# Kernel tuning notes

Hardware: AMD Instinct MI355X
Metric: run time of the kernel (lower is better)

Reference implementation:

```python
import jax, jax.numpy as jnp
import numpy as np
import math

N_NODES = 50000
N_EDGES = 800000
F_IN = 32
HID = 64


def _layernorm(x, g, b, eps=1e-5):
    mu = x.mean(-1, keepdims=True)
    var = ((x - mu) ** 2).mean(-1, keepdims=True)
    return (x - mu) / jnp.sqrt(var + eps) * g + b


def _tconv(x, src, dst, Wq, bq, Wk, bk, Wv, bv, Ws, heads):
    # PyG TransformerConv (concat=True, root_weight=True, bias=False on skip)
    N = x.shape[0]
    C = Wq.shape[1] // heads
    q = (x @ Wq + bq).reshape(N, heads, C)[dst]  # [E,H,C] gathered at targets
    k = (x @ Wk + bk).reshape(N, heads, C)[src]  # [E,H,C] gathered at sources
    v = (x @ Wv + bv).reshape(N, heads, C)[src]
    scores = (q * k).sum(-1) / math.sqrt(C)      # [E,H]
    m = jax.ops.segment_max(scores, dst, num_segments=N)   # [N,H]
    p = jnp.exp(scores - m[dst])
    denom = jax.ops.segment_sum(p, dst, num_segments=N)
    alpha = p / (denom[dst] + 1e-16)             # segment softmax over in-edges
    agg = jax.ops.segment_sum(v * alpha[..., None], dst, num_segments=N)
    return agg.reshape(N, heads * C) + x @ Ws    # + skip (no bias)


def setup_inputs() -> dict:
    key = jax.random.key(0)
    ks = iter(jax.random.split(key, 64))
    def rn(shape, s=0.1):
        return jax.random.normal(next(ks), shape, jnp.float32) * s
    inp = {
        "x": rn((N_NODES, F_IN), 1.0),
        "edge_index": jax.random.randint(next(ks), (2, N_EDGES), 0, N_NODES, dtype=jnp.int32),
        "ln0_g": jnp.ones((F_IN,), jnp.float32),
        "ln0_b": jnp.zeros((F_IN,), jnp.float32),
    }
    dims = [F_IN, HID, HID]
    for l in range(3):
        d = dims[l]
        inp[f"Wq{l}"] = rn((d, HID)); inp[f"bq{l}"] = rn((HID,), 0.05)
        inp[f"Wk{l}"] = rn((d, HID)); inp[f"bk{l}"] = rn((HID,), 0.05)
        inp[f"Wv{l}"] = rn((d, HID)); inp[f"bv{l}"] = rn((HID,), 0.05)
        inp[f"Ws{l}"] = rn((d, HID))
        inp[f"g{l}"] = jnp.ones((HID,), jnp.float32)
        inp[f"b{l}"] = jnp.zeros((HID,), jnp.float32)
    inp["Wr1"] = rn((HID, HID // 2)); inp["br1"] = jnp.zeros((HID // 2,), jnp.float32)
    inp["Wr2"] = rn((HID // 2, 1));   inp["br2"] = jnp.zeros((1,), jnp.float32)
    inp["Wt1"] = rn((HID, HID // 2)); inp["bt1"] = jnp.zeros((HID // 2,), jnp.float32)
    inp["Wt2"] = rn((HID // 2, 1));   inp["bt2"] = jnp.zeros((1,), jnp.float32)
    return inp


def reference(x, edge_index, ln0_g, ln0_b,
              Wq0, bq0, Wk0, bk0, Wv0, bv0, Ws0, g0, b0,
              Wq1, bq1, Wk1, bk1, Wv1, bv1, Ws1, g1, b1,
              Wq2, bq2, Wk2, bk2, Wv2, bv2, Ws2, g2, b2,
              Wr1, br1, Wr2, br2, Wt1, bt1, Wt2, bt2):
    src, dst = edge_index[0], edge_index[1]
    h = _layernorm(x, ln0_g, ln0_b)
    layers = [
        (Wq0, bq0, Wk0, bk0, Wv0, bv0, Ws0, g0, b0, 4),
        (Wq1, bq1, Wk1, bk1, Wv1, bv1, Ws1, g1, b1, 4),
        (Wq2, bq2, Wk2, bk2, Wv2, bv2, Ws2, g2, b2, 1),
    ]
    for i, (Wq, bq, Wk, bk, Wv, bv, Ws, g, b, heads) in enumerate(layers):
        x_res = h if h.shape[-1] == HID else None
        h = _tconv(h, src, dst, Wq, bq, Wk, bk, Wv, bv, Ws, heads)
        h = _layernorm(h, g, b)
        if x_res is not None and i > 0:
            h = h + 0.1 * x_res
        if i < len(layers) - 1:
            h = jax.nn.relu(h)  # dropout is identity in eval mode
    rtt = jax.nn.relu(h @ Wr1 + br1) @ Wr2 + br2      # [N,1]
    retrans = jax.nn.relu(h @ Wt1 + bt1) @ Wt2 + bt2  # [N,1]
    return jnp.concatenate([rtt, retrans], axis=1)    # [N,2]
```

## Files before the change

### kernel.cpp

```cpp
#include <hip/hip_runtime.h>
#include <hip/hip_bf16.h>
#include <math.h>

#define N_NODES 50000
#define N_EDGES 800000
#define HID 64
#define NBK 196
#define EPB 1024
#define SB  ((N_EDGES + EPB - 1) / EPB)
#define FLAT (NBK * SB)
#define SCAN_B ((FLAT + 255) / 256)

#define QKVS0_BLKS 3125

#define LN0_BLKS   6250
#define HIST_BLKS  SB
#define WP0_BLKS   32
#define WP12_BLKS  64
#define PREP_BLKS  (LN0_BLKS + HIST_BLKS + WP0_BLKS + 2 * WP12_BLKS)

typedef __attribute__((ext_vector_type(8))) short short8;
typedef __attribute__((ext_vector_type(4))) float float4v;

__device__ __forceinline__ unsigned short f32_to_bf16_rne(float f) {
    unsigned int u = __float_as_uint(f);
    unsigned int r = u + 0x7fffu + ((u >> 16) & 1u);
    return (unsigned short)(r >> 16);
}

__device__ __forceinline__ void ln0_body(int b, int t,
        const float* __restrict__ x, const float* __restrict__ g,
        const float* __restrict__ bb, float* __restrict__ h0) {
    int lane = t & 63;
    int n = b * 8 + (t >> 6) * 2 + (lane >> 5);
    int c = lane & 31;
    float v = x[n * 32 + c];
    float s = v;
    #pragma unroll
    for (int off = 1; off < 32; off <<= 1) s += __shfl_xor(s, off);
    float mu = s * (1.0f / 32.0f);
    float d = v - mu;
    float vs = d * d;
    #pragma unroll
    for (int off = 1; off < 32; off <<= 1) vs += __shfl_xor(vs, off);
    float var = vs * (1.0f / 32.0f);
    h0[n * 32 + c] = d * rsqrtf(var + 1e-5f) * g[c] + bb[c];
}

__device__ __forceinline__ void wprep_body(int idx, int KS,
        const float* __restrict__ Wq, const float* __restrict__ Wk,
        const float* __restrict__ Wv, const float* __restrict__ Ws,
        unsigned short* __restrict__ Wp) {
    int j = idx & 7;
    int lane = (idx >> 3) & 63;
    int ts = idx >> 9;
    int s = ts % KS;
    int tile = ts / KS;
    int which = tile >> 2;
    int slice = tile & 3;
    int k = s * 32 + ((lane >> 4) * 8) + j;
    int col = slice * 16 + (lane & 15);
    const float* W = (which == 0) ? Wq : (which == 1) ? Wk : (which == 2) ? Wv : Ws;
    Wp[idx] = f32_to_bf16_rne(W[k * 64 + col]);
}

__global__ __launch_bounds__(256) void prep_kernel(
        const float* __restrict__ x, const float* __restrict__ ln0g,
        const float* __restrict__ ln0b, float* __restrict__ h0,
        const int* __restrict__ dst, int* __restrict__ ghist,
        const float* __restrict__ Wq0, const float* __restrict__ Wk0,
        const float* __restrict__ Wv0, const float* __restrict__ Ws0,
        unsigned short* __restrict__ Wp0,
        const float* __restrict__ Wq1, const float* __restrict__ Wk1,
        const float* __restrict__ Wv1, const float* __restrict__ Ws1,
        unsigned short* __restrict__ Wp1,
        const float* __restrict__ Wq2, const float* __restrict__ Wk2,
        const float* __restrict__ Wv2, const float* __restrict__ Ws2,
        unsigned short* __restrict__ Wp2) {
    __shared__ int hist[NBK];
    int b = blockIdx.x;
    int t = threadIdx.x;
    if (b < LN0_BLKS) {
        ln0_body(b, t, x, ln0g, ln0b, h0);
    } else if (b < LN0_BLKS + HIST_BLKS) {
        int i = b - LN0_BLKS;
        for (int k = t; k < NBK; k += 256) hist[k] = 0;
        __syncthreads();
        int e0 = i * EPB;
        #pragma unroll
        for (int r = 0; r < EPB / 256; r++) {
            int e = e0 + r * 256 + t;
            if (e < N_EDGES) atomicAdd(&hist[dst[e] >> 8], 1);
        }
        __syncthreads();
        for (int k = t; k < NBK; k += 256) ghist[k * SB + i] = hist[k];
    } else if (b < LN0_BLKS + HIST_BLKS + WP0_BLKS) {
        int idx = (b - LN0_BLKS - HIST_BLKS) * 256 + t;
        wprep_body(idx, 1, Wq0, Wk0, Wv0, Ws0, Wp0);
    } else if (b < LN0_BLKS + HIST_BLKS + WP0_BLKS + WP12_BLKS) {
        int idx = (b - LN0_BLKS - HIST_BLKS - WP0_BLKS) * 256 + t;
        wprep_body(idx, 2, Wq1, Wk1, Wv1, Ws1, Wp1);
    } else {
        int idx = (b - LN0_BLKS - HIST_BLKS - WP0_BLKS - WP12_BLKS) * 256 + t;
        wprep_body(idx, 2, Wq2, Wk2, Wv2, Ws2, Wp2);
    }
}

__global__ void scan1_kernel(const int* __restrict__ ghist, int* __restrict__ csum) {
    int f = blockIdx.x * 256 + threadIdx.x;
    int v = (f < FLAT) ? ghist[f] : 0;
    #pragma unroll
    for (int off = 1; off < 64; off <<= 1) v += __shfl_xor(v, off);
    __shared__ int ws[4];
    if ((threadIdx.x & 63) == 0) ws[threadIdx.x >> 6] = v;
    __syncthreads();
    if (threadIdx.x == 0) csum[blockIdx.x] = ws[0] + ws[1] + ws[2] + ws[3];
}

__global__ void scan2_kernel(const int* __restrict__ csum, int* __restrict__ coff,
                             int* __restrict__ bbase, int* __restrict__ row_ptr) {
    int lane = threadIdx.x;
    int carry = 0;
    for (int base = 0; base < SCAN_B; base += 64) {
        int i = base + lane;
        int v = (i < SCAN_B) ? csum[i] : 0;
        int incl = v;
        #pragma unroll
        for (int off = 1; off < 64; off <<= 1) {
            int tt = __shfl_up(incl, off);
            if (lane >= off) incl += tt;
        }
        if (i < SCAN_B) coff[i] = carry + incl - v;
        carry += __shfl(incl, 63);
    }
    if (lane == 0) { bbase[NBK] = N_EDGES; row_ptr[N_NODES] = N_EDGES; }
}

__global__ void scan3_kernel(const int* __restrict__ ghist, const int* __restrict__ coff,
                             int* __restrict__ goff, int* __restrict__ bbase) {
    int f = blockIdx.x * 256 + threadIdx.x;
    int lane = threadIdx.x & 63;
    int w = threadIdx.x >> 6;
    int v = (f < FLAT) ? ghist[f] : 0;
    int incl = v;
    #pragma unroll
    for (int off = 1; off < 64; off <<= 1) {
        int tt = __shfl_up(incl, off);
        if (lane >= off) incl += tt;
    }
    __shared__ int ws[4];
    if (lane == 63) ws[w] = incl;
    __syncthreads();
    int woff = 0;
    #pragma unroll
    for (int k = 0; k < 4; k++) if (k < w) woff += ws[k];
    int excl = coff[blockIdx.x] + woff + incl - v;
    if (f < FLAT) {
        goff[f] = excl;
        if (f % SB == 0) bbase[f / SB] = excl;
    }
}

template <int D>
__device__ __forceinline__ void qkvs_body(int bid, int t,
        const float* __restrict__ h,
        const unsigned short* __restrict__ Wp,
        const float* __restrict__ bq, const float* __restrict__ bk,
        const float* __restrict__ bv, float scale,
        unsigned int* __restrict__ QS, unsigned int* __restrict__ KV) {
    constexpr int KS = D / 32;
    int lane = t & 63;
    int w = t >> 6;
    int n0 = bid * 16;
    int n16 = lane & 15;
    int quad = lane >> 4;
    int col = w * 16 + n16;

    short8 afrag[KS];
    #pragma unroll
    for (int s = 0; s < KS; s++) {
        const float* hp = &h[(n0 + n16) * D + s * 32 + quad * 8];
        float4 a0 = *(const float4*)hp;
        float4 a1 = *(const float4*)(hp + 4);
        short8 af;
        af[0] = (short)f32_to_bf16_rne(a0.x);
        af[1] = (short)f32_to_bf16_rne(a0.y);
        af[2] = (short)f32_to_bf16_rne(a0.z);
        af[3] = (short)f32_to_bf16_rne(a0.w);
        af[4] = (short)f32_to_bf16_rne(a1.x);
        af[5] = (short)f32_to_bf16_rne(a1.y);
        af[6] = (short)f32_to_bf16_rne(a1.z);
        af[7] = (short)f32_to_bf16_rne(a1.w);
        afrag[s] = af;
    }

    float4v accs[4];
    #pragma unroll
    for (int which = 0; which < 4; which++) {
        float4v acc = {0.0f, 0.0f, 0.0f, 0.0f};
        int tile = which * 4 + w;
        #pragma unroll
        for (int s = 0; s < KS; s++) {
            short8 bfrag = *(const short8*)&Wp[((tile * KS + s) * 64 + lane) * 8];
            acc = __builtin_amdgcn_mfma_f32_16x16x32_bf16(afrag[s], bfrag, acc, 0, 0, 0);
        }
        accs[which] = acc;
    }

    float bqc = bq[col], bkc = bk[col], bvc = bv[col];

    #pragma unroll
    for (int r = 0; r < 4; r++) {
        int node = n0 + quad * 4 + r;
        unsigned int qw = f32_to_bf16_rne((accs[0][r] + bqc) * scale);
        unsigned int kw = f32_to_bf16_rne(accs[1][r] + bkc);
        unsigned int vw = f32_to_bf16_rne(accs[2][r] + bvc);
        unsigned int sw = f32_to_bf16_rne(accs[3][r]);
        KV[node * 64 + col] = (vw << 16) | kw;
        QS[node * 64 + col] = (sw << 16) | qw;
    }
}

template <int D>
__global__ __launch_bounds__(256) void qkvs_mfma_kernel(
        const float* __restrict__ h,
        const unsigned short* __restrict__ Wp,
        const float* __restrict__ bq, const float* __restrict__ bk,
        const float* __restrict__ bv, float scale,
        unsigned int* __restrict__ QS, unsigned int* __restrict__ KV) {
    qkvs_body<D>(blockIdx.x, threadIdx.x, h, Wp, bq, bk, bv, scale, QS, KV);
}

__global__ __launch_bounds__(256) void scatter_qkvs0_kernel(
        const int* __restrict__ src, const int* __restrict__ dst,
        const int* __restrict__ goff, int2* __restrict__ ebkt,
        const float* __restrict__ h, const unsigned short* __restrict__ Wp,
        const float* __restrict__ bq, const float* __restrict__ bk,
        const float* __restrict__ bv, float scale,
        unsigned int* __restrict__ QS, unsigned int* __restrict__ KV) {
    __shared__ int hist[NBK];
    int t = threadIdx.x;
    if (blockIdx.x < SB) {
        int i = blockIdx.x;
        for (int k = t; k < NBK; k += 256) hist[k] = 0;
        __syncthreads();
        int e0 = i * EPB;
        #pragma unroll
        for (int r = 0; r < EPB / 256; r++) {
            int e = e0 + r * 256 + t;
            if (e < N_EDGES) {
                int s = src[e], d = dst[e];
                int k = d >> 8;
                int rank = atomicAdd(&hist[k], 1);
                ebkt[goff[k * SB + i] + rank] = make_int2(s, d);
            }
        }
    } else {
        qkvs_body<32>(blockIdx.x - SB, t, h, Wp, bq, bk, bv, scale, QS, KV);
    }
}

__global__ __launch_bounds__(256) void bucket_build_kernel(
        const int2* __restrict__ ebkt, const int* __restrict__ bbase,
        int* __restrict__ row_ptr, int* __restrict__ colb) {
    __shared__ int ldeg[256];
    __shared__ int lcur[256];
    __shared__ int wsum[4];
    int b = blockIdx.x;
    int t = threadIdx.x;
    int cbase = bbase[b];
    int cnt = bbase[b + 1] - cbase;

    ldeg[t] = 0;
    __syncthreads();
    for (int i = t; i < cnt; i += 256) {
        int2 e = ebkt[cbase + i];
        atomicAdd(&ldeg[e.y & 255], 1);
    }
    __syncthreads();

    int lane = t & 63;
    int w = t >> 6;
    int v = ldeg[t];
    int incl = v;
    #pragma unroll
    for (int off = 1; off < 64; off <<= 1) {
        int tt = __shfl_up(incl, off);
        if (lane >= off) incl += tt;
    }
    if (lane == 63) wsum[w] = incl;
    __syncthreads();
    int woff = 0;
    #pragma unroll
    for (int k = 0; k < 4; k++) if (k < w) woff += wsum[k];
    int excl = woff + incl - v;

    int node = b * 256 + t;
    if (node < N_NODES) row_ptr[node] = cbase + excl;
    lcur[t] = excl;
    __syncthreads();

    for (int i = t; i < cnt; i += 256) {
        int2 e = ebkt[cbase + i];
        int r = atomicAdd(&lcur[e.y & 255], 1);
        colb[cbase + r] = e.x;
    }
}

template <int HEADS, bool RES, bool RELU, bool HEAD>
__global__ __launch_bounds__(256) void agg_kernel(
                           const unsigned int* __restrict__ QS,
                           const unsigned int* __restrict__ KV,
                           const int* __restrict__ row_ptr, const int* __restrict__ colb,
                           const float* __restrict__ g, const float* __restrict__ b,
                           const float* __restrict__ h_in, float* __restrict__ h_out,
                           const float* __restrict__ Wr1, const float* __restrict__ br1,
                           const float* __restrict__ Wr2, const float* __restrict__ br2,
                           const float* __restrict__ Wt1, const float* __restrict__ bt1,
                           const float* __restrict__ Wt2, const float* __restrict__ bt2,
                           float* __restrict__ out) {
    constexpr int C = HID / HEADS;
    int lane = threadIdx.x & 63;
    int m = lane & 15;
    int grp = lane >> 4;
    int n = blockIdx.x * 4 + (threadIdx.x >> 6);

    uint4 qs = *(const uint4*)&QS[n * 64 + 4 * m];
    float4 q4 = make_float4(__uint_as_float(qs.x << 16),
                            __uint_as_float(qs.y << 16),
                            __uint_as_float(qs.z << 16),
                            __uint_as_float(qs.w << 16));

    int beg = row_ptr[n], end = row_ptr[n + 1];

    float ssum = 0.0f;
    float acc0 = 0.0f, acc1 = 0.0f, acc2 = 0.0f, acc3 = 0.0f;

    for (int base = beg; base < end; base += 64) {
        int limit = min(end - base, 64);
        int src_l = (base + lane < end) ? colb[base + lane] : 0;
        for (int sub = 0; sub < limit; sub += 16) {
            int e0 = sub + grp, e1 = sub + 4 + grp, e2 = sub + 8 + grp, e3 = sub + 12 + grp;
            int s0 = __shfl(src_l, e0);
            int s1 = __shfl(src_l, e1);
            int s2 = __shfl(src_l, e2);
            int s3 = __shfl(src_l, e3);
            bool v0ok = e0 < limit, v1ok = e1 < limit, v2ok = e2 < limit, v3ok = e3 < limit;
            uint4 kv0 = make_uint4(0, 0, 0, 0), kv1 = kv0, kv2 = kv0, kv3 = kv0;
            if (v0ok) kv0 = *(const uint4*)&KV[(size_t)s0 * 64 + 4 * m];
            if (v1ok) kv1 = *(const uint4*)&KV[(size_t)s1 * 64 + 4 * m];
            if (v2ok) kv2 = *(const uint4*)&KV[(size_t)s2 * 64 + 4 * m];
            if (v3ok) kv3 = *(const uint4*)&KV[(size_t)s3 * 64 + 4 * m];

            float t0 = fmaf(q4.x, __uint_as_float(kv0.x << 16),
                       fmaf(q4.y, __uint_as_float(kv0.y << 16),
                       fmaf(q4.z, __uint_as_float(kv0.z << 16),
                            q4.w * __uint_as_float(kv0.w << 16))));
            float t1 = fmaf(q4.x, __uint_as_float(kv1.x << 16),
                       fmaf(q4.y, __uint_as_float(kv1.y << 16),
                       fmaf(q4.z, __uint_as_float(kv1.z << 16),
                            q4.w * __uint_as_float(kv1.w << 16))));
            float t2 = fmaf(q4.x, __uint_as_float(kv2.x << 16),
                       fmaf(q4.y, __uint_as_float(kv2.y << 16),
                       fmaf(q4.z, __uint_as_float(kv2.z << 16),
                            q4.w * __uint_as_float(kv2.w << 16))));
            float t3 = fmaf(q4.x, __uint_as_float(kv3.x << 16),
                       fmaf(q4.y, __uint_as_float(kv3.y << 16),
                       fmaf(q4.z, __uint_as_float(kv3.z << 16),
                            q4.w * __uint_as_float(kv3.w << 16))));
            #pragma unroll
            for (int off = 1; off < C / 4; off <<= 1) {
                t0 += __shfl_xor(t0, off);
                t1 += __shfl_xor(t1, off);
                t2 += __shfl_xor(t2, off);
                t3 += __shfl_xor(t3, off);
            }
            float p0 = v0ok ? __expf(t0) : 0.0f;
            float p1 = v1ok ? __expf(t1) : 0.0f;
            float p2 = v2ok ? __expf(t2) : 0.0f;
            float p3 = v3ok ? __expf(t3) : 0.0f;
            ssum += (p0 + p1) + (p2 + p3);
            acc0 = fmaf(p0, __uint_as_float(kv0.x & 0xffff0000u),
                   fmaf(p1, __uint_as_float(kv1.x & 0xffff0000u),
                   fmaf(p2, __uint_as_float(kv2.x & 0xffff0000u),
                   fmaf(p3, __uint_as_float(kv3.x & 0xffff0000u), acc0))));
            acc1 = fmaf(p0, __uint_as_float(kv0.y & 0xffff0000u),
                   fmaf(p1, __uint_as_float(kv1.y & 0xffff0000u),
                   fmaf(p2, __uint_as_float(kv2.y & 0xffff0000u),
                   fmaf(p3, __uint_as_float(kv3.y & 0xffff0000u), acc1))));
            acc2 = fmaf(p0, __uint_as_float(kv0.z & 0xffff0000u),
                   fmaf(p1, __uint_as_float(kv1.z & 0xffff0000u),
                   fmaf(p2, __uint_as_float(kv2.z & 0xffff0000u),
                   fmaf(p3, __uint_as_float(kv3.z & 0xffff0000u), acc2))));
            acc3 = fmaf(p0, __uint_as_float(kv0.w & 0xffff0000u),
                   fmaf(p1, __uint_as_float(kv1.w & 0xffff0000u),
                   fmaf(p2, __uint_as_float(kv2.w & 0xffff0000u),
                   fmaf(p3, __uint_as_float(kv3.w & 0xffff0000u), acc3))));
        }
    }

    #pragma unroll
    for (int off = 16; off < 64; off <<= 1) {
        ssum += __shfl_xor(ssum, off);
        acc0 += __shfl_xor(acc0, off);
        acc1 += __shfl_xor(acc1, off);
        acc2 += __shfl_xor(acc2, off);
        acc3 += __shfl_xor(acc3, off);
    }

    float inv = 1.0f / (ssum + 1e-16f);
    float o0 = fmaf(acc0, inv, __uint_as_float(qs.x & 0xffff0000u));
    float o1 = fmaf(acc1, inv, __uint_as_float(qs.y & 0xffff0000u));
    float o2 = fmaf(acc2, inv, __uint_as_float(qs.z & 0xffff0000u));
    float o3 = fmaf(acc3, inv, __uint_as_float(qs.w & 0xffff0000u));

    float s = (o0 + o1) + (o2 + o3);
    #pragma unroll
    for (int off = 1; off < 16; off <<= 1) s += __shfl_xor(s, off);
    float mu = s * (1.0f / 64.0f);
    float d0 = o0 - mu, d1 = o1 - mu, d2 = o2 - mu, d3 = o3 - mu;
    float vs = (d0 * d0 + d1 * d1) + (d2 * d2 + d3 * d3);
    #pragma unroll
    for (int off = 1; off < 16; off <<= 1) vs += __shfl_xor(vs, off);
    float rstd = rsqrtf(vs * (1.0f / 64.0f) + 1e-5f);

    float4 gv = *(const float4*)&g[4 * m];
    float4 bv = *(const float4*)&b[4 * m];
    float y0 = d0 * rstd * gv.x + bv.x;
    float y1 = d1 * rstd * gv.y + bv.y;
    float y2 = d2 * rstd * gv.z + bv.z;
    float y3 = d3 * rstd * gv.w + bv.w;
    if (RES) {
        float4 rv = *(const float4*)&h_in[n * 64 + 4 * m];
        y0 = fmaf(0.1f, rv.x, y0);
        y1 = fmaf(0.1f, rv.y, y1);
        y2 = fmaf(0.1f, rv.z, y2);
        y3 = fmaf(0.1f, rv.w, y3);
    }
    if (RELU) {
        y0 = fmaxf(y0, 0.0f); y1 = fmaxf(y1, 0.0f);
        y2 = fmaxf(y2, 0.0f); y3 = fmaxf(y3, 0.0f);
    }

    if (!HEAD) {
        if (grp == 0) {
            float4 yv = make_float4(y0, y1, y2, y3);
            *(float4*)&h_out[n * 64 + 4 * m] = yv;
        }
    } else {
        __shared__ float sh[4][HID];
        int wave = threadIdx.x >> 6;
        if (grp == 0) {
            float4 yv = make_float4(y0, y1, y2, y3);
            *(float4*)&sh[wave][4 * m] = yv;
        }
        __syncthreads();
        int half = lane >> 5;
        int j = lane & 31;
        const float* W1 = half ? Wt1 : Wr1;
        const float* b1 = half ? bt1 : br1;
        const float* W2 = half ? Wt2 : Wr2;
        const float* b2v = half ? bt2 : br2;
        float a = b1[j];
        #pragma unroll 8
        for (int i = 0; i < 64; i++) a = fmaf(sh[wave][i], W1[i * 32 + j], a);
        a = fmaxf(a, 0.0f);
        float r = a * W2[j];
        #pragma unroll
        for (int off = 1; off < 32; off <<= 1) r += __shfl_xor(r, off);
        if (j == 0) out[n * 2 + half] = r + b2v[0];
    }
}

extern "C" void kernel_launch(void* const* d_in, const int* in_sizes, int n_in,
                              void* d_out, int out_size, void* d_ws, size_t ws_size,
                              hipStream_t stream) {
    const float* x    = (const float*)d_in[0];
    const int*   ei   = (const int*)d_in[1];
    const int*   src  = ei;
    const int*   dst  = ei + N_EDGES;
    const float* ln0g = (const float*)d_in[2];
    const float* ln0b = (const float*)d_in[3];

    const float* P[27];
    for (int i = 0; i < 27; i++) P[i] = (const float*)d_in[4 + i];
    const float* Wr1 = (const float*)d_in[31];
    const float* br1 = (const float*)d_in[32];
    const float* Wr2 = (const float*)d_in[33];
    const float* br2 = (const float*)d_in[34];
    const float* Wt1 = (const float*)d_in[35];
    const float* bt1 = (const float*)d_in[36];
    const float* Wt2 = (const float*)d_in[37];
    const float* bt2 = (const float*)d_in[38];

    float* out = (float*)d_out;

    float* hbuf0 = (float*)d_ws;
    float* hbuf1 = hbuf0 + N_NODES * 64;
    unsigned int* QSb = (unsigned int*)(hbuf1 + N_NODES * 64);
    unsigned int* KVb = QSb + N_NODES * 64;
    int* row_ptr = (int*)(KVb + N_NODES * 64);
    int* colb    = row_ptr + (N_NODES + 1);
    int* ghist   = colb + N_EDGES;
    int* goff    = ghist + FLAT;
    int* csum    = goff + FLAT;
    int* coff    = csum + SCAN_B;
    int* bbase   = coff + SCAN_B;
    unsigned short* Wp0 = (unsigned short*)(bbase + NBK + 1);
    unsigned short* Wp1 = Wp0 + 16 * 1 * 512;
    unsigned short* Wp2 = Wp1 + 16 * 2 * 512;
    int2* ebkt = (int2*)hbuf1;

    prep_kernel<<<PREP_BLKS, 256, 0, stream>>>(x, ln0g, ln0b, hbuf0,
        dst, ghist,
        P[0],  P[2],  P[4],  P[6],  Wp0,
        P[9],  P[11], P[13], P[15], Wp1,
        P[18], P[20], P[22], P[24], Wp2);
    scan1_kernel<<<SCAN_B, 256, 0, stream>>>(ghist, csum);
    scan2_kernel<<<1, 64, 0, stream>>>(csum, coff, bbase, row_ptr);
    scan3_kernel<<<SCAN_B, 256, 0, stream>>>(ghist, coff, goff, bbase);
    scatter_qkvs0_kernel<<<SB + QKVS0_BLKS, 256, 0, stream>>>(src, dst, goff, ebkt,
        hbuf0, Wp0, P[1], P[3], P[5], 0.25f, QSb, KVb);
    bucket_build_kernel<<<NBK, 256, 0, stream>>>(ebkt, bbase, row_ptr, colb);

    agg_kernel<4, false, true, false><<<12500, 256, 0, stream>>>(QSb, KVb,
        row_ptr, colb, P[7], P[8], nullptr, hbuf1,
        Wr1, br1, Wr2, br2, Wt1, bt1, Wt2, bt2, out);

    qkvs_mfma_kernel<64><<<3125, 256, 0, stream>>>(hbuf1, Wp1,
        P[10], P[12], P[14], 0.25f, QSb, KVb);
    agg_kernel<4, true, true, false><<<12500, 256, 0, stream>>>(QSb, KVb,
        row_ptr, colb, P[16], P[17], hbuf1, hbuf0,
        Wr1, br1, Wr2, br2, Wt1, bt1, Wt2, bt2, out);

    qkvs_mfma_kernel<64><<<3125, 256, 0, stream>>>(hbuf0, Wp2,
        P[19], P[21], P[23], 0.125f, QSb, KVb);
    agg_kernel<1, true, false, true><<<12500, 256, 0, stream>>>(QSb, KVb,
        row_ptr, colb, P[25], P[26], hbuf0, hbuf1,
        Wr1, br1, Wr2, br2, Wt1, bt1, Wt2, bt2, out);
}
```

Baseline: 324.4 us.

## Store keys as fp8 and values as fp16, split Q and skip into fp32

The per-node projection layout changes. Keys are packed into fp8 (4 per word) and values into fp16 (4 per uint2), while Q and the skip term move to separate fp32 arrays. The per-edge gathers in the aggregation kernels shrink from 16 bytes to 12 bytes per lane, which cuts the random-access traffic that dominates the edge loop. In exchange, Q/S writes and reads double in size, conversion instructions and cross-lane shuffles are added, and fp8 keys lower attention-score precision, which may exceed tolerance.

```diff
diff --git a/kernel.cpp b/kernel.cpp
--- a/kernel.cpp
+++ b/kernel.cpp
@@ -1,5 +1,6 @@
 #include <hip/hip_runtime.h>
 #include <hip/hip_bf16.h>
+#include <hip/hip_fp16.h>
 #include <math.h>
 
 #define N_NODES 50000
@@ -21,11 +22,24 @@
 
 typedef __attribute__((ext_vector_type(8))) short short8;
 typedef __attribute__((ext_vector_type(4))) float float4v;
+typedef __attribute__((ext_vector_type(2))) float float2v;
 
 __device__ __forceinline__ unsigned short f32_to_bf16_rne(float f) {
     unsigned int u = __float_as_uint(f);
     unsigned int r = u + 0x7fffu + ((u >> 16) & 1u);
     return (unsigned short)(r >> 16);
+}
+
+__device__ __forceinline__ unsigned int f32_to_fp8_byte(float f) {
+    return (unsigned int)__builtin_amdgcn_cvt_pk_fp8_f32(f, f, 0, false) & 0xffu;
+}
+template <bool HI>
+__device__ __forceinline__ float2v fp8x2_to_f32(unsigned int w) {
+    return __builtin_amdgcn_cvt_pk_f32_fp8((int)w, HI);
+}
+__device__ __forceinline__ float2 h2_to_f32(unsigned int w) {
+    __half2 h = *reinterpret_cast<__half2*>(&w);
+    return __half22float2(h);
 }
 
 __device__ __forceinline__ void ln0_body(int b, int t,
@@ -167,7 +181,8 @@
         const unsigned short* __restrict__ Wp,
         const float* __restrict__ bq, const float* __restrict__ bk,
         const float* __restrict__ bv, float scale,
-        unsigned int* __restrict__ QS, unsigned int* __restrict__ KV) {
+        float* __restrict__ Qf, float* __restrict__ Sf,
+        unsigned int* __restrict__ K8, uint2* __restrict__ Vh) {
     constexpr int KS = D / 32;
     int lane = t & 63;
     int w = t >> 6;
@@ -208,16 +223,25 @@
     }
 
     float bqc = bq[col], bkc = bk[col], bvc = bv[col];
+    int j = n16 & 3;
+    int mword = (col >> 2);
 
     #pragma unroll
     for (int r = 0; r < 4; r++) {
         int node = n0 + quad * 4 + r;
-        unsigned int qw = f32_to_bf16_rne((accs[0][r] + bqc) * scale);
-        unsigned int kw = f32_to_bf16_rne(accs[1][r] + bkc);
-        unsigned int vw = f32_to_bf16_rne(accs[2][r] + bvc);
-        unsigned int sw = f32_to_bf16_rne(accs[3][r]);
-        KV[node * 64 + col] = (vw << 16) | kw;
-        QS[node * 64 + col] = (sw << 16) | qw;
+        Qf[node * 64 + col] = (accs[0][r] + bqc) * scale;
+        Sf[node * 64 + col] = accs[3][r];
+        unsigned int ku = f32_to_fp8_byte(accs[1][r] + bkc) << (8 * j);
+        ku |= __shfl_xor(ku, 1); ku |= __shfl_xor(ku, 2);
+        unsigned int hb = (unsigned int)__half_as_ushort(__float2half_rn(accs[2][r] + bvc));
+        unsigned int vx = (j < 2) ? (hb << (16 * j)) : 0u;
+        unsigned int vy = (j >= 2) ? (hb << (16 * (j - 2))) : 0u;
+        vx |= __shfl_xor(vx, 1); vx |= __shfl_xor(vx, 2);
+        vy |= __shfl_xor(vy, 1); vy |= __shfl_xor(vy, 2);
+        if (j == 0) {
+            K8[node * 16 + mword] = ku;
+            Vh[node * 16 + mword] = make_uint2(vx, vy);
+        }
     }
 }
 
@@ -227,8 +251,9 @@
         const unsigned short* __restrict__ Wp,
         const float* __restrict__ bq, const float* __restrict__ bk,
         const float* __restrict__ bv, float scale,
-        unsigned int* __restrict__ QS, unsigned int* __restrict__ KV) {
-    qkvs_body<D>(blockIdx.x, threadIdx.x, h, Wp, bq, bk, bv, scale, QS, KV);
+        float* __restrict__ Qf, float* __restrict__ Sf,
+        unsigned int* __restrict__ K8, uint2* __restrict__ Vh) {
+    qkvs_body<D>(blockIdx.x, threadIdx.x, h, Wp, bq, bk, bv, scale, Qf, Sf, K8, Vh);
 }
 
 __global__ __launch_bounds__(256) void scatter_qkvs0_kernel(
@@ -237,7 +262,8 @@
         const float* __restrict__ h, const unsigned short* __restrict__ Wp,
         const float* __restrict__ bq, const float* __restrict__ bk,
         const float* __restrict__ bv, float scale,
-        unsigned int* __restrict__ QS, unsigned int* __restrict__ KV) {
+        float* __restrict__ Qf, float* __restrict__ Sf,
+        unsigned int* __restrict__ K8, uint2* __restrict__ Vh) {
     __shared__ int hist[NBK];
     int t = threadIdx.x;
     if (blockIdx.x < SB) {
@@ -256,7 +282,7 @@
             }
         }
     } else {
-        qkvs_body<32>(blockIdx.x - SB, t, h, Wp, bq, bk, bv, scale, QS, KV);
+        qkvs_body<32>(blockIdx.x - SB, t, h, Wp, bq, bk, bv, scale, Qf, Sf, K8, Vh);
     }
 }
 
@@ -309,8 +335,10 @@
 
 template <int HEADS, bool RES, bool RELU, bool HEAD>
 __global__ __launch_bounds__(256) void agg_kernel(
-                           const unsigned int* __restrict__ QS,
-                           const unsigned int* __restrict__ KV,
+                           const float* __restrict__ Qf,
+                           const float* __restrict__ Sf,
+                           const unsigned int* __restrict__ K8,
+                           const uint2* __restrict__ Vh,
                            const int* __restrict__ row_ptr, const int* __restrict__ colb,
                            const float* __restrict__ g, const float* __restrict__ b,
                            const float* __restrict__ h_in, float* __restrict__ h_out,
@@ -325,11 +353,7 @@
     int grp = lane >> 4;
     int n = blockIdx.x * 4 + (threadIdx.x >> 6);
 
-    uint4 qs = *(const uint4*)&QS[n * 64 + 4 * m];
-    float4 q4 = make_float4(__uint_as_float(qs.x << 16),
-                            __uint_as_float(qs.y << 16),
-                            __uint_as_float(qs.z << 16),
-                            __uint_as_float(qs.w << 16));
+    float4 q4 = *(const float4*)&Qf[n * 64 + 4 * m];
 
     int beg = row_ptr[n], end = row_ptr[n + 1];
 
@@ -346,28 +370,26 @@
             int s2 = __shfl(src_l, e2);
             int s3 = __shfl(src_l, e3);
             bool v0ok = e0 < limit, v1ok = e1 < limit, v2ok = e2 < limit, v3ok = e3 < limit;
-            uint4 kv0 = make_uint4(0, 0, 0, 0), kv1 = kv0, kv2 = kv0, kv3 = kv0;
-            if (v0ok) kv0 = *(const uint4*)&KV[(size_t)s0 * 64 + 4 * m];
-            if (v1ok) kv1 = *(const uint4*)&KV[(size_t)s1 * 64 + 4 * m];
-            if (v2ok) kv2 = *(const uint4*)&KV[(size_t)s2 * 64 + 4 * m];
-            if (v3ok) kv3 = *(const uint4*)&KV[(size_t)s3 * 64 + 4 * m];
-
-            float t0 = fmaf(q4.x, __uint_as_float(kv0.x << 16),
-                       fmaf(q4.y, __uint_as_float(kv0.y << 16),
-                       fmaf(q4.z, __uint_as_float(kv0.z << 16),
-                            q4.w * __uint_as_float(kv0.w << 16))));
-            float t1 = fmaf(q4.x, __uint_as_float(kv1.x << 16),
-                       fmaf(q4.y, __uint_as_float(kv1.y << 16),
-                       fmaf(q4.z, __uint_as_float(kv1.z << 16),
-                            q4.w * __uint_as_float(kv1.w << 16))));
-            float t2 = fmaf(q4.x, __uint_as_float(kv2.x << 16),
-                       fmaf(q4.y, __uint_as_float(kv2.y << 16),
-                       fmaf(q4.z, __uint_as_float(kv2.z << 16),
-                            q4.w * __uint_as_float(kv2.w << 16))));
-            float t3 = fmaf(q4.x, __uint_as_float(kv3.x << 16),
-                       fmaf(q4.y, __uint_as_float(kv3.y << 16),
-                       fmaf(q4.z, __uint_as_float(kv3.z << 16),
-                            q4.w * __uint_as_float(kv3.w << 16))));
+            unsigned int ka0 = 0, ka1 = 0, ka2 = 0, ka3 = 0;
+            uint2 va0 = make_uint2(0, 0), va1 = va0, va2 = va0, va3 = va0;
+            if (v0ok) { ka0 = K8[(size_t)s0 * 16 + m]; va0 = Vh[(size_t)s0 * 16 + m]; }
+            if (v1ok) { ka1 = K8[(size_t)s1 * 16 + m]; va1 = Vh[(size_t)s1 * 16 + m]; }
+            if (v2ok) { ka2 = K8[(size_t)s2 * 16 + m]; va2 = Vh[(size_t)s2 * 16 + m]; }
+            if (v3ok) { ka3 = K8[(size_t)s3 * 16 + m]; va3 = Vh[(size_t)s3 * 16 + m]; }
+
+            float2v k0a = fp8x2_to_f32<false>(ka0), k0b = fp8x2_to_f32<true>(ka0);
+            float2v k1a = fp8x2_to_f32<false>(ka1), k1b = fp8x2_to_f32<true>(ka1);
+            float2v k2a = fp8x2_to_f32<false>(ka2), k2b = fp8x2_to_f32<true>(ka2);
+            float2v k3a = fp8x2_to_f32<false>(ka3), k3b = fp8x2_to_f32<true>(ka3);
+
+            float t0 = fmaf(q4.x, k0a.x, fmaf(q4.y, k0a.y,
+                       fmaf(q4.z, k0b.x, q4.w * k0b.y)));
+            float t1 = fmaf(q4.x, k1a.x, fmaf(q4.y, k1a.y,
+                       fmaf(q4.z, k1b.x, q4.w * k1b.y)));
+            float t2 = fmaf(q4.x, k2a.x, fmaf(q4.y, k2a.y,
+                       fmaf(q4.z, k2b.x, q4.w * k2b.y)));
+            float t3 = fmaf(q4.x, k3a.x, fmaf(q4.y, k3a.y,
+                       fmaf(q4.z, k3b.x, q4.w * k3b.y)));
             #pragma unroll
             for (int off = 1; off < C / 4; off <<= 1) {
                 t0 += __shfl_xor(t0, off);
@@ -380,22 +402,20 @@
             float p2 = v2ok ? __expf(t2) : 0.0f;
             float p3 = v3ok ? __expf(t3) : 0.0f;
             ssum += (p0 + p1) + (p2 + p3);
-            acc0 = fmaf(p0, __uint_as_float(kv0.x & 0xffff0000u),
-                   fmaf(p1, __uint_as_float(kv1.x & 0xffff0000u),
-                   fmaf(p2, __uint_as_float(kv2.x & 0xffff0000u),
-                   fmaf(p3, __uint_as_float(kv3.x & 0xffff0000u), acc0))));
-            acc1 = fmaf(p0, __uint_as_float(kv0.y & 0xffff0000u),
-                   fmaf(p1, __uint_as_float(kv1.y & 0xffff0000u),
-                   fmaf(p2, __uint_as_float(kv2.y & 0xffff0000u),
-                   fmaf(p3, __uint_as_float(kv3.y & 0xffff0000u), acc1))));
-            acc2 = fmaf(p0, __uint_as_float(kv0.z & 0xffff0000u),
-                   fmaf(p1, __uint_as_float(kv1.z & 0xffff0000u),
-                   fmaf(p2, __uint_as_float(kv2.z & 0xffff0000u),
-                   fmaf(p3, __uint_as_float(kv3.z & 0xffff0000u), acc2))));
-            acc3 = fmaf(p0, __uint_as_float(kv0.w & 0xffff0000u),
-                   fmaf(p1, __uint_as_float(kv1.w & 0xffff0000u),
-                   fmaf(p2, __uint_as_float(kv2.w & 0xffff0000u),
-                   fmaf(p3, __uint_as_float(kv3.w & 0xffff0000u), acc3))));
+
+            float2 v0a = h2_to_f32(va0.x), v0b = h2_to_f32(va0.y);
+            float2 v1a = h2_to_f32(va1.x), v1b = h2_to_f32(va1.y);
+            float2 v2a = h2_to_f32(va2.x), v2b = h2_to_f32(va2.y);
+            float2 v3a = h2_to_f32(va3.x), v3b = h2_to_f32(va3.y);
+
+            acc0 = fmaf(p0, v0a.x, fmaf(p1, v1a.x,
+                   fmaf(p2, v2a.x, fmaf(p3, v3a.x, acc0))));
+            acc1 = fmaf(p0, v0a.y, fmaf(p1, v1a.y,
+                   fmaf(p2, v2a.y, fmaf(p3, v3a.y, acc1))));
+            acc2 = fmaf(p0, v0b.x, fmaf(p1, v1b.x,
+                   fmaf(p2, v2b.x, fmaf(p3, v3b.x, acc2))));
+            acc3 = fmaf(p0, v0b.y, fmaf(p1, v1b.y,
+                   fmaf(p2, v2b.y, fmaf(p3, v3b.y, acc3))));
         }
     }
 
@@ -409,10 +429,11 @@
     }
 
     float inv = 1.0f / (ssum + 1e-16f);
-    float o0 = fmaf(acc0, inv, __uint_as_float(qs.x & 0xffff0000u));
-    float o1 = fmaf(acc1, inv, __uint_as_float(qs.y & 0xffff0000u));
-    float o2 = fmaf(acc2, inv, __uint_as_float(qs.z & 0xffff0000u));
-    float o3 = fmaf(acc3, inv, __uint_as_float(qs.w & 0xffff0000u));
+    float4 sv = *(const float4*)&Sf[n * 64 + 4 * m];
+    float o0 = fmaf(acc0, inv, sv.x);
+    float o1 = fmaf(acc1, inv, sv.y);
+    float o2 = fmaf(acc2, inv, sv.z);
+    float o3 = fmaf(acc3, inv, sv.w);
 
     float s = (o0 + o1) + (o2 + o3);
     #pragma unroll
@@ -497,9 +518,11 @@
 
     float* hbuf0 = (float*)d_ws;
     float* hbuf1 = hbuf0 + N_NODES * 64;
-    unsigned int* QSb = (unsigned int*)(hbuf1 + N_NODES * 64);
-    unsigned int* KVb = QSb + N_NODES * 64;
-    int* row_ptr = (int*)(KVb + N_NODES * 64);
+    float* Qf    = hbuf1 + N_NODES * 64;
+    float* Sf    = Qf + N_NODES * 64;
+    unsigned int* K8 = (unsigned int*)(Sf + N_NODES * 64);
+    uint2* Vh    = (uint2*)(K8 + N_NODES * 16);
+    int* row_ptr = (int*)(Vh + N_NODES * 16);
     int* colb    = row_ptr + (N_NODES + 1);
     int* ghist   = colb + N_EDGES;
     int* goff    = ghist + FLAT;
@@ -520,22 +543,22 @@
     scan2_kernel<<<1, 64, 0, stream>>>(csum, coff, bbase, row_ptr);
     scan3_kernel<<<SCAN_B, 256, 0, stream>>>(ghist, coff, goff, bbase);
     scatter_qkvs0_kernel<<<SB + QKVS0_BLKS, 256, 0, stream>>>(src, dst, goff, ebkt,
-        hbuf0, Wp0, P[1], P[3], P[5], 0.25f, QSb, KVb);
+        hbuf0, Wp0, P[1], P[3], P[5], 0.25f, Qf, Sf, K8, Vh);
     bucket_build_kernel<<<NBK, 256, 0, stream>>>(ebkt, bbase, row_ptr, colb);
 
-    agg_kernel<4, false, true, false><<<12500, 256, 0, stream>>>(QSb, KVb,
+    agg_kernel<4, false, true, false><<<12500, 256, 0, stream>>>(Qf, Sf, K8, Vh,
         row_ptr, colb, P[7], P[8], nullptr, hbuf1,
         Wr1, br1, Wr2, br2, Wt1, bt1, Wt2, bt2, out);
 
     qkvs_mfma_kernel<64><<<3125, 256, 0, stream>>>(hbuf1, Wp1,
-        P[10], P[12], P[14], 0.25f, QSb, KVb);
-    agg_kernel<4, true, true, false><<<12500, 256, 0, stream>>>(QSb, KVb,
+        P[10], P[12], P[14], 0.25f, Qf, Sf, K8, Vh);
+    agg_kernel<4, true, true, false><<<12500, 256, 0, stream>>>(Qf, Sf, K8, Vh,
         row_ptr, colb, P[16], P[17], hbuf1, hbuf0,
         Wr1, br1, Wr2, br2, Wt1, bt1, Wt2, bt2, out);
 
     qkvs_mfma_kernel<64><<<3125, 256, 0, stream>>>(hbuf0, Wp2,
-        P[19], P[21], P[23], 0.125f, QSb, KVb);
-    agg_kernel<1, true, false, true><<<12500, 256, 0, stream>>>(QSb, KVb,
+        P[19], P[21], P[23], 0.125f, Qf, Sf, K8, Vh);
+    agg_kernel<1, true, false, true><<<12500, 256, 0, stream>>>(Qf, Sf, K8, Vh,
         row_ptr, colb, P[25], P[26], hbuf0, hbuf1,
         Wr1, br1, Wr2, br2, Wt1, bt1, Wt2, bt2, out);
 }
```

Result: no change. 330.1 us (+1.8%).

## Build CSR with per-node global atomic degree and cursor instead of bucketed two-pass sort

Applied to the files above, without the earlier changes.

Replaces the two-level bucket sort CSR build (per-block bucket histograms, scatter into buckets, then per-bucket local sort) with a direct per-node degree count using global atomics, a scan over nodes, and a scatter of sources through per-node atomic cursors. This removes the bucket_build kernel and the intermediate int2 edge buffer. In exchange it uses many contended global atomics and makes the order of neighbors within a row nondeterministic, which can change floating-point summation order. It adds a memset of the degree array and moves a few stores in the qkvs epilogue.

```diff
diff --git a/kernel.cpp b/kernel.cpp
--- a/kernel.cpp
+++ b/kernel.cpp
@@ -5,19 +5,17 @@
 #define N_NODES 50000
 #define N_EDGES 800000
 #define HID 64
-#define NBK 196
 #define EPB 1024
 #define SB  ((N_EDGES + EPB - 1) / EPB)
-#define FLAT (NBK * SB)
-#define SCAN_B ((FLAT + 255) / 256)
+#define NSC 196
 
 #define QKVS0_BLKS 3125
 
 #define LN0_BLKS   6250
-#define HIST_BLKS  SB
+#define DEG_BLKS   SB
 #define WP0_BLKS   32
 #define WP12_BLKS  64
-#define PREP_BLKS  (LN0_BLKS + HIST_BLKS + WP0_BLKS + 2 * WP12_BLKS)
+#define PREP_BLKS  (LN0_BLKS + DEG_BLKS + WP0_BLKS + 2 * WP12_BLKS)
 
 typedef __attribute__((ext_vector_type(8))) short short8;
 typedef __attribute__((ext_vector_type(4))) float float4v;
@@ -67,7 +65,7 @@
 __global__ __launch_bounds__(256) void prep_kernel(
         const float* __restrict__ x, const float* __restrict__ ln0g,
         const float* __restrict__ ln0b, float* __restrict__ h0,
-        const int* __restrict__ dst, int* __restrict__ ghist,
+        const int* __restrict__ dst, int* __restrict__ deg,
         const float* __restrict__ Wq0, const float* __restrict__ Wk0,
         const float* __restrict__ Wv0, const float* __restrict__ Ws0,
         unsigned short* __restrict__ Wp0,
@@ -77,38 +75,33 @@
         const float* __restrict__ Wq2, const float* __restrict__ Wk2,
         const float* __restrict__ Wv2, const float* __restrict__ Ws2,
         unsigned short* __restrict__ Wp2) {
-    __shared__ int hist[NBK];
     int b = blockIdx.x;
     int t = threadIdx.x;
     if (b < LN0_BLKS) {
         ln0_body(b, t, x, ln0g, ln0b, h0);
-    } else if (b < LN0_BLKS + HIST_BLKS) {
+    } else if (b < LN0_BLKS + DEG_BLKS) {
         int i = b - LN0_BLKS;
-        for (int k = t; k < NBK; k += 256) hist[k] = 0;
-        __syncthreads();
         int e0 = i * EPB;
         #pragma unroll
         for (int r = 0; r < EPB / 256; r++) {
             int e = e0 + r * 256 + t;
-            if (e < N_EDGES) atomicAdd(&hist[dst[e] >> 8], 1);
-        }
-        __syncthreads();
-        for (int k = t; k < NBK; k += 256) ghist[k * SB + i] = hist[k];
-    } else if (b < LN0_BLKS + HIST_BLKS + WP0_BLKS) {
-        int idx = (b - LN0_BLKS - HIST_BLKS) * 256 + t;
+            if (e < N_EDGES) atomicAdd(&deg[dst[e]], 1);
+        }
+    } else if (b < LN0_BLKS + DEG_BLKS + WP0_BLKS) {
+        int idx = (b - LN0_BLKS - DEG_BLKS) * 256 + t;
         wprep_body(idx, 1, Wq0, Wk0, Wv0, Ws0, Wp0);
-    } else if (b < LN0_BLKS + HIST_BLKS + WP0_BLKS + WP12_BLKS) {
-        int idx = (b - LN0_BLKS - HIST_BLKS - WP0_BLKS) * 256 + t;
+    } else if (b < LN0_BLKS + DEG_BLKS + WP0_BLKS + WP12_BLKS) {
+        int idx = (b - LN0_BLKS - DEG_BLKS - WP0_BLKS) * 256 + t;
         wprep_body(idx, 2, Wq1, Wk1, Wv1, Ws1, Wp1);
     } else {
-        int idx = (b - LN0_BLKS - HIST_BLKS - WP0_BLKS - WP12_BLKS) * 256 + t;
+        int idx = (b - LN0_BLKS - DEG_BLKS - WP0_BLKS - WP12_BLKS) * 256 + t;
         wprep_body(idx, 2, Wq2, Wk2, Wv2, Ws2, Wp2);
     }
 }
 
-__global__ void scan1_kernel(const int* __restrict__ ghist, int* __restrict__ csum) {
-    int f = blockIdx.x * 256 + threadIdx.x;
-    int v = (f < FLAT) ? ghist[f] : 0;
+__global__ void scanA_kernel(const int* __restrict__ deg, int* __restrict__ csum) {
+    int n = blockIdx.x * 256 + threadIdx.x;
+    int v = (n < N_NODES) ? deg[n] : 0;
     #pragma unroll
     for (int off = 1; off < 64; off <<= 1) v += __shfl_xor(v, off);
     __shared__ int ws[4];
@@ -117,31 +110,31 @@
     if (threadIdx.x == 0) csum[blockIdx.x] = ws[0] + ws[1] + ws[2] + ws[3];
 }
 
-__global__ void scan2_kernel(const int* __restrict__ csum, int* __restrict__ coff,
-                             int* __restrict__ bbase, int* __restrict__ row_ptr) {
+__global__ void scanB_kernel(const int* __restrict__ csum, int* __restrict__ coff,
+                             int* __restrict__ row_ptr) {
     int lane = threadIdx.x;
     int carry = 0;
-    for (int base = 0; base < SCAN_B; base += 64) {
+    for (int base = 0; base < NSC; base += 64) {
         int i = base + lane;
-        int v = (i < SCAN_B) ? csum[i] : 0;
+        int v = (i < NSC) ? csum[i] : 0;
         int incl = v;
         #pragma unroll
         for (int off = 1; off < 64; off <<= 1) {
             int tt = __shfl_up(incl, off);
             if (lane >= off) incl += tt;
         }
-        if (i < SCAN_B) coff[i] = carry + incl - v;
+        if (i < NSC) coff[i] = carry + incl - v;
         carry += __shfl(incl, 63);
     }
-    if (lane == 0) { bbase[NBK] = N_EDGES; row_ptr[N_NODES] = N_EDGES; }
-}
-
-__global__ void scan3_kernel(const int* __restrict__ ghist, const int* __restrict__ coff,
-                             int* __restrict__ goff, int* __restrict__ bbase) {
-    int f = blockIdx.x * 256 + threadIdx.x;
+    if (lane == 0) row_ptr[N_NODES] = N_EDGES;
+}
+
+__global__ void scanC_kernel(const int* __restrict__ deg, const int* __restrict__ coff,
+                             int* __restrict__ row_ptr, int* __restrict__ cur) {
+    int n = blockIdx.x * 256 + threadIdx.x;
     int lane = threadIdx.x & 63;
     int w = threadIdx.x >> 6;
-    int v = (f < FLAT) ? ghist[f] : 0;
+    int v = (n < N_NODES) ? deg[n] : 0;
     int incl = v;
     #pragma unroll
     for (int off = 1; off < 64; off <<= 1) {
@@ -155,9 +148,9 @@
     #pragma unroll
     for (int k = 0; k < 4; k++) if (k < w) woff += ws[k];
     int excl = coff[blockIdx.x] + woff + incl - v;
-    if (f < FLAT) {
-        goff[f] = excl;
-        if (f % SB == 0) bbase[f / SB] = excl;
+    if (n < N_NODES) {
+        row_ptr[n] = excl;
+        cur[n] = excl;
     }
 }
 
@@ -213,11 +206,11 @@
     for (int r = 0; r < 4; r++) {
         int node = n0 + quad * 4 + r;
         unsigned int qw = f32_to_bf16_rne((accs[0][r] + bqc) * scale);
+        unsigned int sw = f32_to_bf16_rne(accs[3][r]);
+        QS[node * 64 + col] = (sw << 16) | qw;
         unsigned int kw = f32_to_bf16_rne(accs[1][r] + bkc);
         unsigned int vw = f32_to_bf16_rne(accs[2][r] + bvc);
-        unsigned int sw = f32_to_bf16_rne(accs[3][r]);
         KV[node * 64 + col] = (vw << 16) | kw;
-        QS[node * 64 + col] = (sw << 16) | qw;
     }
 }
 
@@ -233,77 +226,25 @@
 
 __global__ __launch_bounds__(256) void scatter_qkvs0_kernel(
         const int* __restrict__ src, const int* __restrict__ dst,
-        const int* __restrict__ goff, int2* __restrict__ ebkt,
+        int* __restrict__ cur, int* __restrict__ colb,
         const float* __restrict__ h, const unsigned short* __restrict__ Wp,
         const float* __restrict__ bq, const float* __restrict__ bk,
         const float* __restrict__ bv, float scale,
         unsigned int* __restrict__ QS, unsigned int* __restrict__ KV) {
-    __shared__ int hist[NBK];
     int t = threadIdx.x;
     if (blockIdx.x < SB) {
-        int i = blockIdx.x;
-        for (int k = t; k < NBK; k += 256) hist[k] = 0;
-        __syncthreads();
-        int e0 = i * EPB;
+        int e0 = blockIdx.x * EPB;
         #pragma unroll
         for (int r = 0; r < EPB / 256; r++) {
             int e = e0 + r * 256 + t;
             if (e < N_EDGES) {
                 int s = src[e], d = dst[e];
-                int k = d >> 8;
-                int rank = atomicAdd(&hist[k], 1);
-                ebkt[goff[k * SB + i] + rank] = make_int2(s, d);
+                int slot = atomicAdd(&cur[d], 1);
+                colb[slot] = s;
             }
         }
     } else {
         qkvs_body<32>(blockIdx.x - SB, t, h, Wp, bq, bk, bv, scale, QS, KV);
-    }
-}
-
-__global__ __launch_bounds__(256) void bucket_build_kernel(
-        const int2* __restrict__ ebkt, const int* __restrict__ bbase,
-        int* __restrict__ row_ptr, int* __restrict__ colb) {
-    __shared__ int ldeg[256];
-    __shared__ int lcur[256];
-    __shared__ int wsum[4];
-    int b = blockIdx.x;
-    int t = threadIdx.x;
-    int cbase = bbase[b];
-    int cnt = bbase[b + 1] - cbase;
-
-    ldeg[t] = 0;
-    __syncthreads();
-    for (int i = t; i < cnt; i += 256) {
-        int2 e = ebkt[cbase + i];
-        atomicAdd(&ldeg[e.y & 255], 1);
-    }
-    __syncthreads();
-
-    int lane = t & 63;
-    int w = t >> 6;
-    int v = ldeg[t];
-    int incl = v;
-    #pragma unroll
-    for (int off = 1; off < 64; off <<= 1) {
-        int tt = __shfl_up(incl, off);
-        if (lane >= off) incl += tt;
-    }
-    if (lane == 63) wsum[w] = incl;
-    __syncthreads();
-    int woff = 0;
-    #pragma unroll
-    for (int k = 0; k < 4; k++) if (k < w) woff += wsum[k];
-    int excl = woff + incl - v;
-
-    int node = b * 256 + t;
-    if (node < N_NODES) row_ptr[node] = cbase + excl;
-    lcur[t] = excl;
-    __syncthreads();
-
-    for (int i = t; i < cnt; i += 256) {
-        int2 e = ebkt[cbase + i];
-        int r = atomicAdd(&lcur[e.y & 255], 1);
-        colb[cbase + r] = e.x;
     }
 }
 
@@ -500,28 +441,27 @@
     unsigned int* QSb = (unsigned int*)(hbuf1 + N_NODES * 64);
     unsigned int* KVb = QSb + N_NODES * 64;
     int* row_ptr = (int*)(KVb + N_NODES * 64);
-    int* colb    = row_ptr + (N_NODES + 1);
-    int* ghist   = colb + N_EDGES;
-    int* goff    = ghist + FLAT;
-    int* csum    = goff + FLAT;
-    int* coff    = csum + SCAN_B;
-    int* bbase   = coff + SCAN_B;
-    unsigned short* Wp0 = (unsigned short*)(bbase + NBK + 1);
+    int* cur     = row_ptr + (N_NODES + 1);
+    int* colb    = cur + N_NODES;
+    int* deg     = colb + N_EDGES;
+    int* csum    = deg + N_NODES;
+    int* coff    = csum + NSC;
+    unsigned short* Wp0 = (unsigned short*)(coff + NSC);
     unsigned short* Wp1 = Wp0 + 16 * 1 * 512;
     unsigned short* Wp2 = Wp1 + 16 * 2 * 512;
-    int2* ebkt = (int2*)hbuf1;
+
+    hipMemsetAsync(deg, 0, N_NODES * sizeof(int), stream);
 
     prep_kernel<<<PREP_BLKS, 256, 0, stream>>>(x, ln0g, ln0b, hbuf0,
-        dst, ghist,
+        dst, deg,
         P[0],  P[2],  P[4],  P[6],  Wp0,
         P[9],  P[11], P[13], P[15], Wp1,
         P[18], P[20], P[22], P[24], Wp2);
-    scan1_kernel<<<SCAN_B, 256, 0, stream>>>(ghist, csum);
-    scan2_kernel<<<1, 64, 0, stream>>>(csum, coff, bbase, row_ptr);
-    scan3_kernel<<<SCAN_B, 256, 0, stream>>>(ghist, coff, goff, bbase);
-    scatter_qkvs0_kernel<<<SB + QKVS0_BLKS, 256, 0, stream>>>(src, dst, goff, ebkt,
+    scanA_kernel<<<NSC, 256, 0, stream>>>(deg, csum);
+    scanB_kernel<<<1, 64, 0, stream>>>(csum, coff, row_ptr);
+    scanC_kernel<<<NSC, 256, 0, stream>>>(deg, coff, row_ptr, cur);
+    scatter_qkvs0_kernel<<<SB + QKVS0_BLKS, 256, 0, stream>>>(src, dst, cur, colb,
         hbuf0, Wp0, P[1], P[3], P[5], 0.25f, QSb, KVb);
-    bucket_build_kernel<<<NBK, 256, 0, stream>>>(ebkt, bbase, row_ptr, colb);
 
     agg_kernel<4, false, true, false><<<12500, 256, 0, stream>>>(QSb, KVb,
         row_ptr, colb, P[7], P[8], nullptr, hbuf1,
```

Result: slower. 386.8 us (+19.2%).

## Split 4-head aggregation into per-head/half-graph blocks plus separate layernorm kernel

Applied to the files above, without the earlier changes.

Replaces the fused 4-head aggregate+layernorm kernel for layers 0 and 1 with a head-partitioned aggregation kernel and a separate layernorm kernel. Each block handles one head of 16 nodes in one half of the node range, so concurrent blocks gather a narrower 64-byte slice of KV. That is meant to improve cache locality and raise parallelism. The softmax skips the max subtraction. The cost is an extra kernel launch and a round trip of the 64-wide output through global memory, plus the risk of exp overflow without the max shift.

```diff
diff --git a/kernel.cpp b/kernel.cpp
--- a/kernel.cpp
+++ b/kernel.cpp
@@ -12,6 +12,10 @@
 #define SCAN_B ((FLAT + 255) / 256)
 
 #define QKVS0_BLKS 3125
+
+#define NHALF 25000
+#define NBH ((NHALF + 15) / 16)
+#define AGGH_BLKS (NBH * 8)
 
 #define LN0_BLKS   6250
 #define HIST_BLKS  SB
@@ -213,11 +217,11 @@
     for (int r = 0; r < 4; r++) {
         int node = n0 + quad * 4 + r;
         unsigned int qw = f32_to_bf16_rne((accs[0][r] + bqc) * scale);
+        unsigned int sw = f32_to_bf16_rne(accs[3][r]);
+        QS[node * 64 + col] = (sw << 16) | qw;
         unsigned int kw = f32_to_bf16_rne(accs[1][r] + bkc);
         unsigned int vw = f32_to_bf16_rne(accs[2][r] + bvc);
-        unsigned int sw = f32_to_bf16_rne(accs[3][r]);
         KV[node * 64 + col] = (vw << 16) | kw;
-        QS[node * 64 + col] = (sw << 16) | qw;
     }
 }
 
@@ -305,6 +309,78 @@
         int r = atomicAdd(&lcur[e.y & 255], 1);
         colb[cbase + r] = e.x;
     }
+}
+
+__global__ __launch_bounds__(256) void agg_head_kernel(
+        const unsigned int* __restrict__ QS,
+        const unsigned int* __restrict__ KV,
+        const int* __restrict__ row_ptr, const int* __restrict__ colb,
+        float* __restrict__ O) {
+    int b = blockIdx.x;
+    int part = b & 7;
+    int h = part >> 1;
+    int half = part & 1;
+    int bi = b >> 3;
+    int t = threadIdx.x;
+    int grp = t >> 4;
+    int m = t & 15;
+    int nl = bi * 16 + grp;
+    if (nl >= NHALF) return;
+    int n = half * NHALF + nl;
+
+    unsigned int qsw = QS[(size_t)n * 64 + h * 16 + m];
+    float q = __uint_as_float(qsw << 16);
+
+    int beg = row_ptr[n], end = row_ptr[n + 1];
+
+    float ssum = 0.0f, acc = 0.0f;
+
+    for (int e = beg; e < end; e += 2) {
+        int i1 = min(e + 1, end - 1);
+        bool ok1 = (e + 1) < end;
+        int s0 = colb[e];
+        int s1 = colb[i1];
+        unsigned int kv0 = KV[(size_t)s0 * 64 + h * 16 + m];
+        unsigned int kv1 = KV[(size_t)s1 * 64 + h * 16 + m];
+        float t0 = q * __uint_as_float(kv0 << 16);
+        float t1 = q * __uint_as_float(kv1 << 16);
+        #pragma unroll
+        for (int off = 1; off < 16; off <<= 1) {
+            t0 += __shfl_xor(t0, off);
+            t1 += __shfl_xor(t1, off);
+        }
+        float p0 = __expf(t0);
+        float p1 = ok1 ? __expf(t1) : 0.0f;
+        ssum += p0 + p1;
+        acc = fmaf(p0, __uint_as_float(kv0 & 0xffff0000u), acc);
+        acc = fmaf(p1, __uint_as_float(kv1 & 0xffff0000u), acc);
+    }
+
+    float inv = 1.0f / (ssum + 1e-16f);
+    O[(size_t)n * 64 + h * 16 + m] = fmaf(acc, inv, __uint_as_float(qsw & 0xffff0000u));
+}
+
+template <bool RES, bool RELU>
+__global__ __launch_bounds__(256) void ln_kernel(
+        float* __restrict__ O,
+        const float* __restrict__ g, const float* __restrict__ b,
+        const float* __restrict__ h_in) {
+    int lane = threadIdx.x & 63;
+    int n = blockIdx.x * 4 + (threadIdx.x >> 6);
+    float o = O[(size_t)n * 64 + lane];
+    float s = o;
+    #pragma unroll
+    for (int off = 1; off < 64; off <<= 1) s += __shfl_xor(s, off);
+    float mu = s * (1.0f / 64.0f);
+    float d = o - mu;
+    float vs = d * d;
+    #pragma unroll
+    for (int off = 1; off < 64; off <<= 1) vs += __shfl_xor(vs, off);
+    float rstd = rsqrtf(vs * (1.0f / 64.0f) + 1e-5f);
+    float y = d * rstd * g[lane] + b[lane];
+    if (RES) y = fmaf(0.1f, h_in[(size_t)n * 64 + lane], y);
+    if (RELU) y = fmaxf(y, 0.0f);
+    O[(size_t)n * 64 + lane] = y;
 }
 
 template <int HEADS, bool RES, bool RELU, bool HEAD>
@@ -523,15 +599,13 @@
         hbuf0, Wp0, P[1], P[3], P[5], 0.25f, QSb, KVb);
     bucket_build_kernel<<<NBK, 256, 0, stream>>>(ebkt, bbase, row_ptr, colb);
 
-    agg_kernel<4, false, true, false><<<12500, 256, 0, stream>>>(QSb, KVb,
-        row_ptr, colb, P[7], P[8], nullptr, hbuf1,
-        Wr1, br1, Wr2, br2, Wt1, bt1, Wt2, bt2, out);
+    agg_head_kernel<<<AGGH_BLKS, 256, 0, stream>>>(QSb, KVb, row_ptr, colb, hbuf1);
+    ln_kernel<false, true><<<12500, 256, 0, stream>>>(hbuf1, P[7], P[8], nullptr);
 
     qkvs_mfma_kernel<64><<<3125, 256, 0, stream>>>(hbuf1, Wp1,
         P[10], P[12], P[14], 0.25f, QSb, KVb);
-    agg_kernel<4, true, true, false><<<12500, 256, 0, stream>>>(QSb, KVb,
-        row_ptr, colb, P[16], P[17], hbuf1, hbuf0,
-        Wr1, br1, Wr2, br2, Wt1, bt1, Wt2, bt2, out);
+    agg_head_kernel<<<AGGH_BLKS, 256, 0, stream>>>(QSb, KVb, row_ptr, colb, hbuf0);
+    ln_kernel<true, true><<<12500, 256, 0, stream>>>(hbuf0, P[16], P[17], hbuf1);
 
     qkvs_mfma_kernel<64><<<3125, 256, 0, stream>>>(hbuf0, Wp2,
         P[19], P[21], P[23], 0.125f, QSb, KVb);
```

Result: slower. 412.8 us (+27.3%).
